# Kernel optimization log

Hardware: AMD Instinct MI355X
Metric: run time of the kernel (lower is better)

The kernel has to match this reference:

```python
import jax, jax.numpy as jnp
import numpy as np

T, B, E, H, HID, SIG = 1024, 4, 1024, 16, 1024, 64


def setup_inputs() -> dict:
    key = jax.random.key(0)
    ks = jax.random.split(key, 16)
    sc = 0.02
    return {
        "x": jax.random.normal(ks[0], (T, B, E), jnp.float32),
        "Wq": jax.random.normal(ks[1], (E, E), jnp.float32) * sc,
        "bq": jnp.zeros((E,), jnp.float32),
        "Wk": jax.random.normal(ks[2], (E, E), jnp.float32) * sc,
        "bk": jnp.zeros((E,), jnp.float32),
        "Wv": jax.random.normal(ks[3], (E, E), jnp.float32) * sc,
        "bv": jnp.zeros((E,), jnp.float32),
        "Wo": jax.random.normal(ks[4], (E, E), jnp.float32) * sc,
        "bo": jnp.zeros((E,), jnp.float32),
        "W1": jax.random.normal(ks[5], (HID, E), jnp.float32) * sc,
        "b1": jnp.zeros((HID,), jnp.float32),
        "W2": jax.random.normal(ks[6], (SIG, HID), jnp.float32) * sc,
        "b2": jnp.zeros((SIG,), jnp.float32),
        "head_signatures": jax.random.normal(ks[7], (H, SIG), jnp.float32),
    }


def reference(x, Wq, bq, Wk, bk, Wv, bv, Wo, bo, W1, b1, W2, b2, head_signatures):
    # x: (T, B, E) fairseq layout; self-attention, no mask, eval mode (no dropout)
    T_, B_, E_ = x.shape
    H_ = head_signatures.shape[0]
    d = E_ // H_
    scaling = d ** -0.5

    q = (x @ Wq.T + bq) * scaling            # (T,B,E)
    k = x @ Wk.T + bk
    v = x @ Wv.T + bv

    def split_heads(z):                        # (T,B,E) -> (B,H,T,d)
        return z.reshape(T_, B_, H_, d).transpose(1, 2, 0, 3)

    qh, kh, vh = split_heads(q), split_heads(k), split_heads(v)

    scores = jnp.einsum("bhtd,bhsd->bhts", qh, kh)   # (B,H,T,T)
    attn = jax.nn.softmax(scores, axis=-1)
    o = jnp.einsum("bhts,bhsd->bhtd", attn, vh)      # (B,H,T,d)

    # head-competition gate: signature MLP on x, match against head signatures,
    # softmax over heads ('softmax' competition type)
    t = jax.nn.relu(x @ W1.T + b1) @ W2.T + b2       # (T,B,SIG)
    logits = t @ head_signatures.T                   # (T,B,H)
    gate = jax.nn.softmax(logits, axis=-1)
    gate = gate.transpose(1, 2, 0)                   # (B,H,T)

    o = o * gate[..., None]                          # gate per-head outputs
    out = o.transpose(2, 0, 1, 3).reshape(T_, B_, E_)  # (T,B,E)
    return out @ Wo.T + bo
```

## Files before the change

kernel.cpp:

```cpp
#include <hip/hip_runtime.h>

#define Tn   1024
#define Bn   4
#define En   1024
#define Hn   16
#define HIDn 1024
#define SIGn 64
#define Mn   (Tn * Bn)

typedef short  s8x8  __attribute__((ext_vector_type(8)));
typedef float  f32x4 __attribute__((ext_vector_type(4)));

__device__ __forceinline__ float bf2f(unsigned short u) {
    return __uint_as_float(((unsigned int)u) << 16);
}
__device__ __forceinline__ unsigned short f2bf(float f) {
    unsigned int x = __float_as_uint(f);
    unsigned int r = (x + 0x7fffu + ((x >> 16) & 1u)) >> 16;
    return (unsigned short)r;
}
__device__ __forceinline__ float exp2asm(float x) {
    float r;
    asm("v_exp_f32 %0, %1" : "=v"(r) : "v"(x));
    return r;
}
__device__ __forceinline__ unsigned int cvtpk(float a, float b) {
    unsigned int r;
    asm("v_cvt_pk_bf16_f32 %0, %1, %2" : "=v"(r) : "v"(a), "v"(b));
    return r;
}

__device__ __forceinline__ void gload_lds16(const void* g, void* l) {
    __builtin_amdgcn_global_load_lds(
        (const __attribute__((address_space(1))) unsigned int*)g,
        (__attribute__((address_space(3))) unsigned int*)l, 16, 0, 0);
}

__global__ __launch_bounds__(256) void cast_bf16(
    const float* __restrict__ s, unsigned short* __restrict__ d, int n8)
{
    int i = blockIdx.x * 256 + threadIdx.x;
    if (i >= n8) return;
    const float4* p = (const float4*)(s + (size_t)i * 8);
    float4 a = p[0], b = p[1];
    s8x8 o;
    o[0] = (short)f2bf(a.x); o[1] = (short)f2bf(a.y);
    o[2] = (short)f2bf(a.z); o[3] = (short)f2bf(a.w);
    o[4] = (short)f2bf(b.x); o[5] = (short)f2bf(b.y);
    o[6] = (short)f2bf(b.z); o[7] = (short)f2bf(b.w);
    *(s8x8*)(d + (size_t)i * 8) = o;
}

__global__ __launch_bounds__(256) void cast_w4(
    const float* __restrict__ W1, const float* __restrict__ Wq,
    const float* __restrict__ Wk, const float* __restrict__ Wv,
    unsigned short* __restrict__ Wcat)
{
    const size_t WELEM = (size_t)En * En;
    int y = blockIdx.y;
    const float* src = (y == 0) ? W1 : (y == 1) ? Wq : (y == 2) ? Wk : Wv;
    unsigned short* dst = Wcat + (size_t)y * WELEM;
    int i = blockIdx.x * 256 + threadIdx.x;
    const float4* p = (const float4*)(src + (size_t)i * 8);
    float4 a = p[0], b = p[1];
    s8x8 o;
    o[0] = (short)f2bf(a.x); o[1] = (short)f2bf(a.y);
    o[2] = (short)f2bf(a.z); o[3] = (short)f2bf(a.w);
    o[4] = (short)f2bf(b.x); o[5] = (short)f2bf(b.y);
    o[6] = (short)f2bf(b.z); o[7] = (short)f2bf(b.w);
    *(s8x8*)(dst + (size_t)i * 8) = o;
}

__global__ __launch_bounds__(256) void bias_concat(
    const float* __restrict__ b1, const float* __restrict__ bq,
    const float* __restrict__ bk, const float* __restrict__ bv,
    float* __restrict__ bcat)
{
    int i = blockIdx.x * 256 + threadIdx.x;
    int w = i >> 10;
    const float* s = (w == 0) ? b1 : (w == 1) ? bq : (w == 2) ? bk : bv;
    bcat[i] = s[i & 1023];
}

template <int PRE>
__global__ __launch_bounds__(256) void fused_proj(
    const float* __restrict__ X, const unsigned short* __restrict__ Xb,
    const unsigned short* __restrict__ Wcat, const float* __restrict__ bcat,
    unsigned short* __restrict__ t1b, unsigned short* __restrict__ qb,
    unsigned short* __restrict__ kb, unsigned short* __restrict__ vb)
{
    __shared__ __align__(16) short As[128 * 32];
    __shared__ __align__(16) short Bs[128 * 32];
    const int tid  = threadIdx.x;
    const int wave = tid >> 6;
    const int lane = tid & 63;
    const int ln15 = lane & 15;
    const int kq   = lane >> 4;
    const int wr   = wave >> 1;
    const int wc   = wave & 1;
    const int bn   = blockIdx.x;
    const int bm   = blockIdx.y;
    const size_t rowA0 = (size_t)bm * 128;
    const size_t rowB0 = (size_t)bn * 128;

    const int lrow   = lane >> 2;
    const int lchunk = lane & 3;

    f32x4 acc[4][4];
#pragma unroll
    for (int m = 0; m < 4; m++)
#pragma unroll
        for (int n = 0; n < 4; n++) acc[m][n] = (f32x4){0.f, 0.f, 0.f, 0.f};

    for (int k0 = 0; k0 < 1024; k0 += 32) {
#pragma unroll
        for (int i = 0; i < 2; i++) {
            int row = wave * 32 + i * 16 + lrow;
            int c   = lchunk ^ ((row >> 1) & 3);
            gload_lds16(Wcat + (rowB0 + row) * 1024 + k0 + c * 8,
                        &Bs[(wave * 32 + i * 16) * 32]);
        }
        if (PRE) {
#pragma unroll
            for (int i = 0; i < 2; i++) {
                int row = wave * 32 + i * 16 + lrow;
                int c   = lchunk ^ ((row >> 1) & 3);
                gload_lds16(Xb + (rowA0 + row) * 1024 + k0 + c * 8,
                            &As[(wave * 32 + i * 16) * 32]);
            }
        } else {
            const int srow = tid >> 1;
            const int scol = (tid & 1) * 16;
            const float4* src = (const float4*)(X + (rowA0 + srow) * 1024 + k0 + scol);
            float4 a = src[0], b = src[1], c4 = src[2], d4 = src[3];
            s8x8 v0, v1;
            v0[0] = (short)f2bf(a.x);  v0[1] = (short)f2bf(a.y);
            v0[2] = (short)f2bf(a.z);  v0[3] = (short)f2bf(a.w);
            v0[4] = (short)f2bf(b.x);  v0[5] = (short)f2bf(b.y);
            v0[6] = (short)f2bf(b.z);  v0[7] = (short)f2bf(b.w);
            v1[0] = (short)f2bf(c4.x); v1[1] = (short)f2bf(c4.y);
            v1[2] = (short)f2bf(c4.z); v1[3] = (short)f2bf(c4.w);
            v1[4] = (short)f2bf(d4.x); v1[5] = (short)f2bf(d4.y);
            v1[6] = (short)f2bf(d4.z); v1[7] = (short)f2bf(d4.w);
            int sw = (srow >> 1) & 3;
            int c0 = (scol >> 3) ^ sw;
            int c1 = ((scol >> 3) + 1) ^ sw;
            *(s8x8*)&As[srow * 32 + c0 * 8] = v0;
            *(s8x8*)&As[srow * 32 + c1 * 8] = v1;
        }
        asm volatile("s_waitcnt vmcnt(0)" ::: "memory");
        __syncthreads();

        s8x8 af[4], bf[4];
#pragma unroll
        for (int m = 0; m < 4; m++) {
            int row = wr * 64 + m * 16 + ln15;
            af[m] = *(const s8x8*)&As[row * 32 + (kq ^ ((row >> 1) & 3)) * 8];
        }
#pragma unroll
        for (int n = 0; n < 4; n++) {
            int row = wc * 64 + n * 16 + ln15;
            bf[n] = *(const s8x8*)&Bs[row * 32 + (kq ^ ((row >> 1) & 3)) * 8];
        }
#pragma unroll
        for (int m = 0; m < 4; m++)
#pragma unroll
            for (int n = 0; n < 4; n++)
                acc[m][n] = __builtin_amdgcn_mfma_f32_16x16x32_bf16(
                    af[m], bf[n], acc[m][n], 0, 0, 0);
        __syncthreads();
    }

    const int which = bn >> 3;
    unsigned short* dst = (which == 0) ? t1b : (which == 1) ? qb
                        : (which == 2) ? kb : vb;
    const float scale = (which == 1) ? 0.18033688011112042f : 1.0f;
    const int   relu  = (which == 0);
    const int   cbase = (bn & 7) * 128;

    float bcol[4];
#pragma unroll
    for (int n = 0; n < 4; n++)
        bcol[n] = bcat[bn * 128 + wc * 64 + n * 16 + ln15];
#pragma unroll
    for (int m = 0; m < 4; m++) {
        size_t gr0 = rowA0 + wr * 64 + m * 16 + kq * 4;
#pragma unroll
        for (int n = 0; n < 4; n++) {
            int gc = cbase + wc * 64 + n * 16 + ln15;
#pragma unroll
            for (int j = 0; j < 4; j++) {
                float vv = acc[m][n][j] + bcol[n];
                if (relu) vv = fmaxf(vv, 0.f);
                vv *= scale;
                dst[(gr0 + j) * 1024 + gc] = f2bf(vv);
            }
        }
    }
}

__global__ __launch_bounds__(256) void out_proj(
    const unsigned short* __restrict__ A, const unsigned short* __restrict__ W,
    const float* __restrict__ bias, float* __restrict__ C)
{
    __shared__ __align__(16) short As[64 * 32];
    __shared__ __align__(16) short Bs[128 * 32];
    const int tid  = threadIdx.x;
    const int wave = tid >> 6;
    const int lane = tid & 63;
    const int ln15 = lane & 15;
    const int kq   = lane >> 4;
    const int wr   = wave >> 1;
    const int wc   = wave & 1;
    const size_t rowA0 = (size_t)blockIdx.y * 64;
    const size_t rowB0 = (size_t)blockIdx.x * 128;

    const int lrow   = lane >> 2;
    const int lchunk = lane & 3;

    f32x4 acc[2][4];
#pragma unroll
    for (int m = 0; m < 2; m++)
#pragma unroll
        for (int n = 0; n < 4; n++) acc[m][n] = (f32x4){0.f, 0.f, 0.f, 0.f};

    for (int k0 = 0; k0 < 1024; k0 += 32) {
        {
            int row = wave * 16 + lrow;
            int c   = lchunk ^ ((row >> 1) & 3);
            gload_lds16(A + (rowA0 + row) * 1024 + k0 + c * 8,
                        &As[(wave * 16) * 32]);
        }
#pragma unroll
        for (int i = 0; i < 2; i++) {
            int row = wave * 32 + i * 16 + lrow;
            int c   = lchunk ^ ((row >> 1) & 3);
            gload_lds16(W + (rowB0 + row) * 1024 + k0 + c * 8,
                        &Bs[(wave * 32 + i * 16) * 32]);
        }
        asm volatile("s_waitcnt vmcnt(0)" ::: "memory");
        __syncthreads();

        s8x8 af[2], bf[4];
#pragma unroll
        for (int m = 0; m < 2; m++) {
            int row = wr * 32 + m * 16 + ln15;
            af[m] = *(const s8x8*)&As[row * 32 + (kq ^ ((row >> 1) & 3)) * 8];
        }
#pragma unroll
        for (int n = 0; n < 4; n++) {
            int row = wc * 64 + n * 16 + ln15;
            bf[n] = *(const s8x8*)&Bs[row * 32 + (kq ^ ((row >> 1) & 3)) * 8];
        }
#pragma unroll
        for (int m = 0; m < 2; m++)
#pragma unroll
            for (int n = 0; n < 4; n++)
                acc[m][n] = __builtin_amdgcn_mfma_f32_16x16x32_bf16(
                    af[m], bf[n], acc[m][n], 0, 0, 0);
        __syncthreads();
    }

    float bcol[4];
#pragma unroll
    for (int n = 0; n < 4; n++)
        bcol[n] = bias[rowB0 + wc * 64 + n * 16 + ln15];
#pragma unroll
    for (int m = 0; m < 2; m++) {
        size_t gr0 = rowA0 + wr * 32 + m * 16 + kq * 4;
#pragma unroll
        for (int n = 0; n < 4; n++) {
            size_t gc = rowB0 + wc * 64 + n * 16 + ln15;
#pragma unroll
            for (int j = 0; j < 4; j++)
                C[(gr0 + j) * 1024 + gc] = acc[m][n][j] + bcol[n];
        }
    }
}

__global__ __launch_bounds__(256) void t2gate(
    const unsigned short* __restrict__ t1, const unsigned short* __restrict__ W2b,
    const float* __restrict__ b2, const float* __restrict__ hs,
    float* __restrict__ gate)
{
    __shared__ __align__(16) short As[16 * 32];
    __shared__ __align__(16) short Bs[64 * 32];
    __shared__ float t2s[16][65];
    __shared__ float hss[16][65];
    const int tid  = threadIdx.x;
    const int wave = tid >> 6;
    const int lane = tid & 63;
    const int ln15 = lane & 15;
    const int kq   = lane >> 4;
    const int m0   = blockIdx.x * 16;

    {
        int r = tid >> 4, c = (tid & 15) * 4;
        float4 v = *(const float4*)(hs + r * 64 + c);
        hss[r][c] = v.x; hss[r][c + 1] = v.y; hss[r][c + 2] = v.z; hss[r][c + 3] = v.w;
    }

    f32x4 acc = (f32x4){0.f, 0.f, 0.f, 0.f};
    for (int k0 = 0; k0 < 1024; k0 += 32) {
        if (tid < 64) {
            int row = tid >> 2, ch = tid & 3;
            int cs = ch ^ ((row >> 1) & 3);
            s8x8 vA = *(const s8x8*)(t1 + (size_t)(m0 + row) * 1024 + k0 + ch * 8);
            *(s8x8*)&As[row * 32 + cs * 8] = vA;
        }
        {
            int row = tid >> 2, ch = tid & 3;
            int cs = ch ^ ((row >> 1) & 3);
            s8x8 vB = *(const s8x8*)(W2b + (size_t)row * 1024 + k0 + ch * 8);
            *(s8x8*)&Bs[row * 32 + cs * 8] = vB;
        }
        __syncthreads();
        int arow = ln15;
        int brow = wave * 16 + ln15;
        s8x8 af = *(const s8x8*)&As[arow * 32 + (kq ^ ((arow >> 1) & 3)) * 8];
        s8x8 bf = *(const s8x8*)&Bs[brow * 32 + (kq ^ ((brow >> 1) & 3)) * 8];
        acc = __builtin_amdgcn_mfma_f32_16x16x32_bf16(af, bf, acc, 0, 0, 0);
        __syncthreads();
    }

#pragma unroll
    for (int j = 0; j < 4; j++)
        t2s[kq * 4 + j][wave * 16 + ln15] = acc[j] + b2[wave * 16 + ln15];
    __syncthreads();

    int r = tid >> 4, hd = tid & 15;
    float s = 0.f;
#pragma unroll 16
    for (int d = 0; d < 64; d++) s += t2s[r][d] * hss[hd][d];
    float mx = s;
    mx = fmaxf(mx, __shfl_xor(mx, 1));
    mx = fmaxf(mx, __shfl_xor(mx, 2));
    mx = fmaxf(mx, __shfl_xor(mx, 4));
    mx = fmaxf(mx, __shfl_xor(mx, 8));
    float e = __expf(s - mx);
    float sum = e;
    sum += __shfl_xor(sum, 1);
    sum += __shfl_xor(sum, 2);
    sum += __shfl_xor(sum, 4);
    sum += __shfl_xor(sum, 8);
    gate[(size_t)(m0 + r) * Hn + hd] = e / sum;
}

__global__ __launch_bounds__(256) void transpose_v(
    const unsigned short* __restrict__ vb, unsigned short* __restrict__ vt)
{
    __shared__ unsigned short ts[64][65];
    const int bh = blockIdx.x;
    const int b = bh >> 4, h = bh & 15;
    const int t0 = blockIdx.y * 64;
    const int tid = threadIdx.x;
    {
        int tr = tid >> 2, dq = (tid & 3) * 16;
        const unsigned short* src =
            vb + ((size_t)(t0 + tr) * Bn + b) * En + h * 64 + dq;
        s8x8 a = *(const s8x8*)src;
        s8x8 c = *(const s8x8*)(src + 8);
#pragma unroll
        for (int i = 0; i < 8; i++) {
            ts[tr][dq + i]     = (unsigned short)a[i];
            ts[tr][dq + 8 + i] = (unsigned short)c[i];
        }
    }
    __syncthreads();
    {
        int dr = tid >> 2, tq = (tid & 3) * 16;
        unsigned short* dst = vt + ((size_t)bh * 64 + dr) * Tn + t0 + tq;
        s8x8 o0, o1;
#pragma unroll
        for (int i = 0; i < 8; i++) {
            o0[i] = (short)ts[tq + i][dr];
            o1[i] = (short)ts[tq + 8 + i][dr];
        }
        *(s8x8*)dst = o0;
        *(s8x8*)(dst + 8) = o1;
    }
}

__global__ __launch_bounds__(256, 5) void attn_mfma(
    const unsigned short* __restrict__ q, const unsigned short* __restrict__ k,
    const unsigned short* __restrict__ vt, const float* __restrict__ gate,
    unsigned short* __restrict__ o)
{
    __shared__ __align__(16) short Kls[2][64 * 64];
    __shared__ __align__(16) short Vls[2][64 * 64];

    const int tid  = threadIdx.x;
    const int w    = tid >> 6;
    const int lane = tid & 63;
    const int ln   = lane & 15;
    const int kq   = lane >> 4;
    const int bh   = blockIdx.x;
    const int b    = bh >> 4;
    const int h    = bh & 15;
    const int qt   = blockIdx.y;

    s8x8 qf[2];
    {
        const int qrow = qt * 64 + w * 16 + ln;
        const unsigned short* src =
            q + ((size_t)qrow * Bn + b) * En + h * 64 + kq * 8;
        qf[0] = *(const s8x8*)(src);
        qf[1] = *(const s8x8*)(src + 32);
    }

    f32x4 OT[4];
#pragma unroll
    for (int n = 0; n < 4; n++) OT[n] = (f32x4){0.f, 0.f, 0.f, 0.f};
    float mrun = -1e30f, lrun = 0.f;

    const int srow0 = w * 16 + (lane >> 3);

    auto stage = [&](int bufi, int s0) {
#pragma unroll
        for (int i = 0; i < 2; i++) {
            int row = srow0 + i * 8;
            int c   = (lane & 7) ^ (row & 7);
            int sK  = 32 * (w >> 1) + 4 * (w & 1)
                    + 8 * ((row >> 2) & 3) + (row & 3);
            const unsigned short* gk =
                k + ((size_t)(s0 + sK) * Bn + b) * En + h * 64 + c * 8;
            gload_lds16(gk, &Kls[bufi][w * 1024 + i * 512]);
            const unsigned short* gv =
                vt + ((size_t)bh * 64 + row) * Tn + s0 + c * 8;
            gload_lds16(gv, &Vls[bufi][w * 1024 + i * 512]);
        }
    };

    stage(0, 0);
    asm volatile("s_waitcnt vmcnt(0)" ::: "memory");
    __syncthreads();

    int cur = 0;
    for (int t = 0; t < Tn / 64; t++) {
        if (t + 1 < Tn / 64) stage(cur ^ 1, (t + 1) * 64);

        f32x4 S[4];
#pragma unroll
        for (int n = 0; n < 4; n++) {
            S[n] = (f32x4){0.f, 0.f, 0.f, 0.f};
#pragma unroll
            for (int kk = 0; kk < 2; kk++) {
                int row = n * 16 + ln;
                int cc  = (kk * 4 + kq) ^ (row & 7);
                s8x8 kf = *(const s8x8*)&Kls[cur][row * 64 + cc * 8];
                S[n] = __builtin_amdgcn_mfma_f32_16x16x32_bf16(kf, qf[kk], S[n], 0, 0, 0);
            }
        }

        float rm;
        {
            f32x4 t0 = S[0];
#pragma unroll
            for (int n = 1; n < 4; n++) {
                t0[0] = fmaxf(t0[0], S[n][0]); t0[1] = fmaxf(t0[1], S[n][1]);
                t0[2] = fmaxf(t0[2], S[n][2]); t0[3] = fmaxf(t0[3], S[n][3]);
            }
            rm = fmaxf(fmaxf(t0[0], t0[1]), fmaxf(t0[2], t0[3]));
            rm = fmaxf(rm, __shfl_xor(rm, 16));
            rm = fmaxf(rm, __shfl_xor(rm, 32));
        }

        if (__any(rm > mrun + 8.0f)) {
            float mnew = fmaxf(mrun, rm);
            float fs = exp2asm(mrun - mnew);
            lrun *= fs;
#pragma unroll
            for (int n = 0; n < 4; n++) {
                OT[n][0] *= fs; OT[n][1] *= fs; OT[n][2] *= fs; OT[n][3] *= fs;
            }
            mrun = mnew;
        }

        float ps = 0.f;
#pragma unroll
        for (int n = 0; n < 4; n++) {
            S[n][0] = exp2asm(S[n][0] - mrun); ps += S[n][0];
            S[n][1] = exp2asm(S[n][1] - mrun); ps += S[n][1];
            S[n][2] = exp2asm(S[n][2] - mrun); ps += S[n][2];
            S[n][3] = exp2asm(S[n][3] - mrun); ps += S[n][3];
        }
        ps += __shfl_xor(ps, 16);
        ps += __shfl_xor(ps, 32);
        lrun += ps;

        union { unsigned int u[4]; s8x8 v; } pb[2];
#pragma unroll
        for (int kk = 0; kk < 2; kk++) {
            pb[kk].u[0] = cvtpk(S[2 * kk][0],     S[2 * kk][1]);
            pb[kk].u[1] = cvtpk(S[2 * kk][2],     S[2 * kk][3]);
            pb[kk].u[2] = cvtpk(S[2 * kk + 1][0], S[2 * kk + 1][1]);
            pb[kk].u[3] = cvtpk(S[2 * kk + 1][2], S[2 * kk + 1][3]);
        }

#pragma unroll
        for (int kk = 0; kk < 2; kk++) {
#pragma unroll
            for (int n = 0; n < 4; n++) {
                int row = n * 16 + ln;
                int cv  = (kk * 4 + kq) ^ (row & 7);
                s8x8 vf = *(const s8x8*)&Vls[cur][row * 64 + cv * 8];
                OT[n] = __builtin_amdgcn_mfma_f32_16x16x32_bf16(vf, pb[kk].v, OT[n], 0, 0, 0);
            }
        }

        asm volatile("s_waitcnt vmcnt(0)" ::: "memory");
        __syncthreads();
        cur ^= 1;
    }

    {
        int tq = qt * 64 + w * 16 + ln;
        size_t m = (size_t)tq * Bn + b;
        float g = gate[m * Hn + h] / lrun;
        unsigned short* dst = o + m * En + h * 64;
#pragma unroll
        for (int n = 0; n < 4; n++) {
            int d0 = n * 16 + kq * 4;
            uint2 pkv;
            pkv.x = cvtpk(OT[n][0] * g, OT[n][1] * g);
            pkv.y = cvtpk(OT[n][2] * g, OT[n][3] * g);
            *(uint2*)(dst + d0) = pkv;
        }
    }
}

extern "C" void kernel_launch(void* const* d_in, const int* in_sizes, int n_in,
                              void* d_out, int out_size, void* d_ws, size_t ws_size,
                              hipStream_t stream)
{
    const float* x  = (const float*)d_in[0];
    const float* Wq = (const float*)d_in[1];
    const float* bq = (const float*)d_in[2];
    const float* Wk = (const float*)d_in[3];
    const float* bk = (const float*)d_in[4];
    const float* Wv = (const float*)d_in[5];
    const float* bv = (const float*)d_in[6];
    const float* Wo = (const float*)d_in[7];
    const float* bo = (const float*)d_in[8];
    const float* W1 = (const float*)d_in[9];
    const float* b1 = (const float*)d_in[10];
    const float* W2 = (const float*)d_in[11];
    const float* b2 = (const float*)d_in[12];
    const float* hs = (const float*)d_in[13];

    const size_t WELEM = (size_t)En * En;
    unsigned short* Wcat = (unsigned short*)d_ws;
    unsigned short* W2b  = Wcat + 4 * WELEM;
    float* bcat = (float*)(W2b + (size_t)SIGn * HIDn);
    float* gate = bcat + 4096;
    unsigned short* t1b = (unsigned short*)(gate + (size_t)Mn * Hn);
    unsigned short* qb  = t1b + (size_t)Mn * En;
    unsigned short* kb  = qb  + (size_t)Mn * En;
    unsigned short* vb  = kb  + (size_t)Mn * En;
    unsigned short* xb  = vb  + (size_t)Mn * En;
    unsigned short* Wob = Wcat;
    unsigned short* vtb = t1b;
    unsigned short* ob  = vb;

    const size_t need_xb =
        (size_t)((char*)(xb + (size_t)Mn * En) - (char*)d_ws);
    const bool pre = ws_size >= need_xb;

    dim3 blk(256);
    const int castGrid = (int)(WELEM / 8 / 256);

    cast_w4<<<dim3(castGrid, 4), blk, 0, stream>>>(W1, Wq, Wk, Wv, Wcat);
    cast_bf16<<<32, blk, 0, stream>>>(W2, W2b, (int)((size_t)SIGn * HIDn / 8));
    bias_concat<<<16, blk, 0, stream>>>(b1, bq, bk, bv, bcat);

    if (pre) {
        cast_bf16<<<dim3((int)((size_t)Mn * En / 8 / 256)), blk, 0, stream>>>(
            x, xb, (int)((size_t)Mn * En / 8));
        fused_proj<1><<<dim3(32, 32), blk, 0, stream>>>(
            x, xb, Wcat, bcat, t1b, qb, kb, vb);
    } else {
        fused_proj<0><<<dim3(32, 32), blk, 0, stream>>>(
            x, xb, Wcat, bcat, t1b, qb, kb, vb);
    }

    t2gate<<<dim3(Mn / 16), blk, 0, stream>>>(t1b, W2b, b2, hs, gate);

    transpose_v<<<dim3(Bn * Hn, Tn / 64), blk, 0, stream>>>(vb, vtb);

    cast_bf16<<<castGrid, blk, 0, stream>>>(Wo, Wob, (int)(WELEM / 8));

    attn_mfma<<<dim3(Bn * Hn, Tn / 64), blk, 0, stream>>>(qb, kb, vtb, gate, ob);

    out_proj<<<dim3(En / 128, Mn / 64), blk, 0, stream>>>(ob, Wob, bo, (float*)d_out);
}
```

Baseline: 141.3 us.

## Merge prep kernels, widen attention blocks, and stage t2gate tiles via direct LDS loads

```diff
diff --git a/kernel.cpp b/kernel.cpp
--- a/kernel.cpp
+++ b/kernel.cpp
@@ -11,9 +11,6 @@
 typedef short  s8x8  __attribute__((ext_vector_type(8)));
 typedef float  f32x4 __attribute__((ext_vector_type(4)));
 
-__device__ __forceinline__ float bf2f(unsigned short u) {
-    return __uint_as_float(((unsigned int)u) << 16);
-}
 __device__ __forceinline__ unsigned short f2bf(float f) {
     unsigned int x = __float_as_uint(f);
     unsigned int r = (x + 0x7fffu + ((x >> 16) & 1u)) >> 16;
@@ -36,50 +33,48 @@
         (__attribute__((address_space(3))) unsigned int*)l, 16, 0, 0);
 }
 
-__global__ __launch_bounds__(256) void cast_bf16(
-    const float* __restrict__ s, unsigned short* __restrict__ d, int n8)
-{
-    int i = blockIdx.x * 256 + threadIdx.x;
-    if (i >= n8) return;
-    const float4* p = (const float4*)(s + (size_t)i * 8);
+__device__ __forceinline__ void cast8(const float* s, unsigned short* d) {
+    const float4* p = (const float4*)s;
     float4 a = p[0], b = p[1];
     s8x8 o;
     o[0] = (short)f2bf(a.x); o[1] = (short)f2bf(a.y);
     o[2] = (short)f2bf(a.z); o[3] = (short)f2bf(a.w);
     o[4] = (short)f2bf(b.x); o[5] = (short)f2bf(b.y);
     o[6] = (short)f2bf(b.z); o[7] = (short)f2bf(b.w);
-    *(s8x8*)(d + (size_t)i * 8) = o;
-}
-
-__global__ __launch_bounds__(256) void cast_w4(
-    const float* __restrict__ W1, const float* __restrict__ Wq,
-    const float* __restrict__ Wk, const float* __restrict__ Wv,
-    unsigned short* __restrict__ Wcat)
+    *(s8x8*)d = o;
+}
+
+__global__ __launch_bounds__(256) void prep_all(
+    const float* __restrict__ x,  const float* __restrict__ W1,
+    const float* __restrict__ Wq, const float* __restrict__ Wk,
+    const float* __restrict__ Wv, const float* __restrict__ W2,
+    const float* __restrict__ b1, const float* __restrict__ bq,
+    const float* __restrict__ bk, const float* __restrict__ bv,
+    unsigned short* __restrict__ Wcat, unsigned short* __restrict__ W2b,
+    float* __restrict__ bcat, unsigned short* __restrict__ xb, int pre)
 {
     const size_t WELEM = (size_t)En * En;
-    int y = blockIdx.y;
-    const float* src = (y == 0) ? W1 : (y == 1) ? Wq : (y == 2) ? Wk : Wv;
-    unsigned short* dst = Wcat + (size_t)y * WELEM;
-    int i = blockIdx.x * 256 + threadIdx.x;
-    const float4* p = (const float4*)(src + (size_t)i * 8);
-    float4 a = p[0], b = p[1];
-    s8x8 o;
-    o[0] = (short)f2bf(a.x); o[1] = (short)f2bf(a.y);
-    o[2] = (short)f2bf(a.z); o[3] = (short)f2bf(a.w);
-    o[4] = (short)f2bf(b.x); o[5] = (short)f2bf(b.y);
-    o[6] = (short)f2bf(b.z); o[7] = (short)f2bf(b.w);
-    *(s8x8*)(dst + (size_t)i * 8) = o;
-}
-
-__global__ __launch_bounds__(256) void bias_concat(
-    const float* __restrict__ b1, const float* __restrict__ bq,
-    const float* __restrict__ bk, const float* __restrict__ bv,
-    float* __restrict__ bcat)
-{
-    int i = blockIdx.x * 256 + threadIdx.x;
-    int w = i >> 10;
-    const float* s = (w == 0) ? b1 : (w == 1) ? bq : (w == 2) ? bk : bv;
-    bcat[i] = s[i & 1023];
+    const int y = blockIdx.y, bx = blockIdx.x, tid = threadIdx.x;
+    if (y < 4) {
+        const float* src = (y == 0) ? W1 : (y == 1) ? Wq : (y == 2) ? Wk : Wv;
+        size_t i = (size_t)bx * 256 + tid;
+        cast8(src + i * 8, Wcat + y * WELEM + i * 8);
+    } else if (y == 4) {
+        if (bx < 32) {
+            size_t i = (size_t)bx * 256 + tid;
+            cast8(W2 + i * 8, W2b + i * 8);
+        } else if (bx < 48) {
+            int idx = (bx - 32) * 256 + tid;
+            int w = idx >> 10;
+            const float* s = (w == 0) ? b1 : (w == 1) ? bq : (w == 2) ? bk : bv;
+            bcat[idx] = s[idx & 1023];
+        }
+    } else {
+        if (!pre) return;
+        int q = y - 5;
+        size_t i = (size_t)bx * 256 + tid;
+        cast8(x + q * WELEM + i * 8, xb + q * WELEM + i * 8);
+    }
 }
 
 template <int PRE>
@@ -283,16 +278,18 @@
     const float* __restrict__ b2, const float* __restrict__ hs,
     float* __restrict__ gate)
 {
-    __shared__ __align__(16) short As[16 * 32];
-    __shared__ __align__(16) short Bs[64 * 32];
+    __shared__ __align__(16) short As[16 * 64];
+    __shared__ __align__(16) short Bs[64 * 64];
     __shared__ float t2s[16][65];
     __shared__ float hss[16][65];
-    const int tid  = threadIdx.x;
-    const int wave = tid >> 6;
-    const int lane = tid & 63;
-    const int ln15 = lane & 15;
-    const int kq   = lane >> 4;
-    const int m0   = blockIdx.x * 16;
+    const int tid   = threadIdx.x;
+    const int wave  = tid >> 6;
+    const int lane  = tid & 63;
+    const int ln15  = lane & 15;
+    const int kq    = lane >> 4;
+    const int lrow8 = lane >> 3;
+    const int lch   = lane & 7;
+    const int m0    = blockIdx.x * 16;
 
     {
         int r = tid >> 4, c = (tid & 15) * 4;
@@ -301,25 +298,31 @@
     }
 
     f32x4 acc = (f32x4){0.f, 0.f, 0.f, 0.f};
-    for (int k0 = 0; k0 < 1024; k0 += 32) {
-        if (tid < 64) {
-            int row = tid >> 2, ch = tid & 3;
-            int cs = ch ^ ((row >> 1) & 3);
-            s8x8 vA = *(const s8x8*)(t1 + (size_t)(m0 + row) * 1024 + k0 + ch * 8);
-            *(s8x8*)&As[row * 32 + cs * 8] = vA;
-        }
-        {
-            int row = tid >> 2, ch = tid & 3;
-            int cs = ch ^ ((row >> 1) & 3);
-            s8x8 vB = *(const s8x8*)(W2b + (size_t)row * 1024 + k0 + ch * 8);
-            *(s8x8*)&Bs[row * 32 + cs * 8] = vB;
-        }
+    for (int k0 = 0; k0 < 1024; k0 += 64) {
+        if (wave < 2) {
+            int row = wave * 8 + lrow8;
+            int cg  = lch ^ (row & 7);
+            gload_lds16(t1 + (size_t)(m0 + row) * 1024 + k0 + cg * 8,
+                        &As[(wave * 8) * 64]);
+        }
+#pragma unroll
+        for (int i = 0; i < 2; i++) {
+            int row = wave * 16 + i * 8 + lrow8;
+            int cg  = lch ^ (row & 7);
+            gload_lds16(W2b + (size_t)row * 1024 + k0 + cg * 8,
+                        &Bs[(wave * 16 + i * 8) * 64]);
+        }
+        asm volatile("s_waitcnt vmcnt(0)" ::: "memory");
         __syncthreads();
-        int arow = ln15;
-        int brow = wave * 16 + ln15;
-        s8x8 af = *(const s8x8*)&As[arow * 32 + (kq ^ ((arow >> 1) & 3)) * 8];
-        s8x8 bf = *(const s8x8*)&Bs[brow * 32 + (kq ^ ((brow >> 1) & 3)) * 8];
-        acc = __builtin_amdgcn_mfma_f32_16x16x32_bf16(af, bf, acc, 0, 0, 0);
+
+#pragma unroll
+        for (int kk = 0; kk < 2; kk++) {
+            int arow = ln15;
+            int brow = wave * 16 + ln15;
+            s8x8 af = *(const s8x8*)&As[arow * 64 + (((kk * 4 + kq) ^ (arow & 7)) * 8)];
+            s8x8 bf = *(const s8x8*)&Bs[brow * 64 + (((kk * 4 + kq) ^ (brow & 7)) * 8)];
+            acc = __builtin_amdgcn_mfma_f32_16x16x32_bf16(af, bf, acc, 0, 0, 0);
+        }
         __syncthreads();
     }
 
@@ -346,14 +349,20 @@
     gate[(size_t)(m0 + r) * Hn + hd] = e / sum;
 }
 
-__global__ __launch_bounds__(256) void transpose_v(
-    const unsigned short* __restrict__ vb, unsigned short* __restrict__ vt)
+__global__ __launch_bounds__(256) void trans_wo(
+    const unsigned short* __restrict__ vb, unsigned short* __restrict__ vt,
+    const float* __restrict__ Wo, unsigned short* __restrict__ Wob)
 {
+    const int bx = blockIdx.x, tid = threadIdx.x;
+    if (bx >= 1024) {
+        size_t i = (size_t)(bx - 1024) * 256 + tid;
+        cast8(Wo + i * 8, Wob + i * 8);
+        return;
+    }
     __shared__ unsigned short ts[64][65];
-    const int bh = blockIdx.x;
+    const int bh = bx & 63;
     const int b = bh >> 4, h = bh & 15;
-    const int t0 = blockIdx.y * 64;
-    const int tid = threadIdx.x;
+    const int t0 = (bx >> 6) * 64;
     {
         int tr = tid >> 2, dq = (tid & 3) * 16;
         const unsigned short* src =
@@ -381,7 +390,7 @@
     }
 }
 
-__global__ __launch_bounds__(256, 5) void attn_mfma(
+__global__ __launch_bounds__(512, 2) void attn_mfma(
     const unsigned short* __restrict__ q, const unsigned short* __restrict__ k,
     const unsigned short* __restrict__ vt, const float* __restrict__ gate,
     unsigned short* __restrict__ o)
@@ -401,7 +410,7 @@
 
     s8x8 qf[2];
     {
-        const int qrow = qt * 64 + w * 16 + ln;
+        const int qrow = qt * 128 + w * 16 + ln;
         const unsigned short* src =
             q + ((size_t)qrow * Bn + b) * En + h * 64 + kq * 8;
         qf[0] = *(const s8x8*)(src);
@@ -413,22 +422,19 @@
     for (int n = 0; n < 4; n++) OT[n] = (f32x4){0.f, 0.f, 0.f, 0.f};
     float mrun = -1e30f, lrun = 0.f;
 
-    const int srow0 = w * 16 + (lane >> 3);
+    const int srow = w * 8 + (lane >> 3);
+    const int sch  = (lane & 7) ^ (srow & 7);
+    const int sn  = srow >> 4;
+    const int sK0 = 32 * (sn >> 1) + 4 * (sn & 1)
+                  + 8 * ((srow >> 2) & 3) + (srow & 3);
 
     auto stage = [&](int bufi, int s0) {
-#pragma unroll
-        for (int i = 0; i < 2; i++) {
-            int row = srow0 + i * 8;
-            int c   = (lane & 7) ^ (row & 7);
-            int sK  = 32 * (w >> 1) + 4 * (w & 1)
-                    + 8 * ((row >> 2) & 3) + (row & 3);
-            const unsigned short* gk =
-                k + ((size_t)(s0 + sK) * Bn + b) * En + h * 64 + c * 8;
-            gload_lds16(gk, &Kls[bufi][w * 1024 + i * 512]);
-            const unsigned short* gv =
-                vt + ((size_t)bh * 64 + row) * Tn + s0 + c * 8;
-            gload_lds16(gv, &Vls[bufi][w * 1024 + i * 512]);
-        }
+        const unsigned short* gk =
+            k + ((size_t)(s0 + sK0) * Bn + b) * En + h * 64 + sch * 8;
+        gload_lds16(gk, &Kls[bufi][w * 512]);
+        const unsigned short* gv =
+            vt + ((size_t)bh * 64 + srow) * Tn + s0 + sch * 8;
+        gload_lds16(gv, &Vls[bufi][w * 512]);
     };
 
     stage(0, 0);
@@ -440,6 +446,7 @@
         if (t + 1 < Tn / 64) stage(cur ^ 1, (t + 1) * 64);
 
         f32x4 S[4];
+        __builtin_amdgcn_s_setprio(1);
 #pragma unroll
         for (int n = 0; n < 4; n++) {
             S[n] = (f32x4){0.f, 0.f, 0.f, 0.f};
@@ -451,6 +458,7 @@
                 S[n] = __builtin_amdgcn_mfma_f32_16x16x32_bf16(kf, qf[kk], S[n], 0, 0, 0);
             }
         }
+        __builtin_amdgcn_s_setprio(0);
 
         float rm;
         {
@@ -497,6 +505,7 @@
             pb[kk].u[3] = cvtpk(S[2 * kk + 1][2], S[2 * kk + 1][3]);
         }
 
+        __builtin_amdgcn_s_setprio(1);
 #pragma unroll
         for (int kk = 0; kk < 2; kk++) {
 #pragma unroll
@@ -507,6 +516,7 @@
                 OT[n] = __builtin_amdgcn_mfma_f32_16x16x32_bf16(vf, pb[kk].v, OT[n], 0, 0, 0);
             }
         }
+        __builtin_amdgcn_s_setprio(0);
 
         asm volatile("s_waitcnt vmcnt(0)" ::: "memory");
         __syncthreads();
@@ -514,7 +524,7 @@
     }
 
     {
-        int tq = qt * 64 + w * 16 + ln;
+        int tq = qt * 128 + w * 16 + ln;
         size_t m = (size_t)tq * Bn + b;
         float g = gate[m * Hn + h] / lrun;
         unsigned short* dst = o + m * En + h * 64;
@@ -567,15 +577,11 @@
     const bool pre = ws_size >= need_xb;
 
     dim3 blk(256);
-    const int castGrid = (int)(WELEM / 8 / 256);
-
-    cast_w4<<<dim3(castGrid, 4), blk, 0, stream>>>(W1, Wq, Wk, Wv, Wcat);
-    cast_bf16<<<32, blk, 0, stream>>>(W2, W2b, (int)((size_t)SIGn * HIDn / 8));
-    bias_concat<<<16, blk, 0, stream>>>(b1, bq, bk, bv, bcat);
+
+    prep_all<<<dim3(512, 9), blk, 0, stream>>>(
+        x, W1, Wq, Wk, Wv, W2, b1, bq, bk, bv, Wcat, W2b, bcat, xb, (int)pre);
 
     if (pre) {
-        cast_bf16<<<dim3((int)((size_t)Mn * En / 8 / 256)), blk, 0, stream>>>(
-            x, xb, (int)((size_t)Mn * En / 8));
         fused_proj<1><<<dim3(32, 32), blk, 0, stream>>>(
             x, xb, Wcat, bcat, t1b, qb, kb, vb);
     } else {
@@ -585,11 +591,10 @@
 
     t2gate<<<dim3(Mn / 16), blk, 0, stream>>>(t1b, W2b, b2, hs, gate);
 
-    transpose_v<<<dim3(Bn * Hn, Tn / 64), blk, 0, stream>>>(vb, vtb);
-
-    cast_bf16<<<castGrid, blk, 0, stream>>>(Wo, Wob, (int)(WELEM / 8));
-
-    attn_mfma<<<dim3(Bn * Hn, Tn / 64), blk, 0, stream>>>(qb, kb, vtb, gate, ob);
+    trans_wo<<<dim3(1536), blk, 0, stream>>>(vb, vtb, Wo, Wob);
+
+    attn_mfma<<<dim3(Bn * Hn, Tn / 128), dim3(512), 0, stream>>>(
+        qb, kb, vtb, gate, ob);
 
     out_proj<<<dim3(En / 128, Mn / 64), blk, 0, stream>>>(ob, Wob, bo, (float*)d_out);
 }
```

Result: faster. 124.3 us (-12.0%).
